# Kernel optimization log

Hardware: AMD Instinct MI355X
Metric: run time of the kernel (lower is better)

## Reference

```python
import math
import jax, jax.numpy as jnp
import numpy as np

B, N, T, C, H = 16, 307, 24, 128, 8
D = C // H
FACTOR = 5
S = min(FACTOR * int(np.ceil(np.log(T))), T)   # sample_k (U_part) = 20
U = S                                          # n_top u = 20


def _pos_emb(t_len, c):
    pos = jnp.arange(t_len, dtype=jnp.float32)[:, None]
    div = jnp.exp(jnp.arange(0, c, 2, dtype=jnp.float32) * (-math.log(10000.0) / c))
    pe = jnp.zeros((t_len, c), dtype=jnp.float32)
    pe = pe.at[:, 0::2].set(jnp.sin(pos * div))
    pe = pe.at[:, 1::2].set(jnp.cos(pos * div))
    return pe  # [T, C]


def _layernorm(x, g, b, eps=1e-5):
    m = x.mean(-1, keepdims=True)
    v = ((x - m) ** 2).mean(-1, keepdims=True)
    return (x - m) / jnp.sqrt(v + eps) * g + b


def _forward(query, time_encoder, index_sample,
             emb_minute, emb_hour, emb_weekday, emb_month, emb_year,
             Wq, Wk, Wv, Wo, bo, ff_w1, ff_b1, ff_w2, ff_b2,
             ln1_g, ln1_b, ln2_g, ln2_b):
    # DataEmbedding: x + positional + temporal (dropout = identity in eval)
    pe = _pos_emb(T, C)                                   # [T, C]
    te = (emb_minute[time_encoder[..., 0]] + emb_hour[time_encoder[..., 1]]
          + emb_weekday[time_encoder[..., 2]] + emb_month[time_encoder[..., 3]]
          + emb_year[time_encoder[..., 4]])               # [B, T, C]
    x = query + pe[None, None, :, :] + te[:, None, :, :]  # [B, N, T, C]

    # QKV projections -> [B, H, N, T, D]
    def proj(inp, W):
        return (inp @ W).reshape(B, N, T, H, D).transpose(0, 3, 1, 2, 4)
    Q, K, V = proj(x, Wq), proj(x, Wk), proj(x, Wv)

    # ProbSparse: sample S keys per query position
    K_samp = K[:, :, :, index_sample, :]                  # [B, H, N, T, S, D]
    QK_samp = jnp.einsum('bhntd,bhntsd->bhnts', Q, K_samp)
    M = QK_samp.max(-1) - QK_samp.sum(-1) / S             # [B, H, N, T]
    _, M_top = jax.lax.top_k(M, U)                        # [B, H, N, U]

    Q_red = jnp.take_along_axis(Q, M_top[..., None], axis=3)  # [B, H, N, U, D]
    scores = jnp.einsum('bhnud,bhntd->bhnut', Q_red, K) * (1.0 / math.sqrt(D))
    attn = jax.nn.softmax(scores, axis=-1)
    upd = jnp.einsum('bhnut,bhntd->bhnud', attn, V)       # [B, H, N, U, D]

    # initial context = mean over T, then scatter-update top-u query rows
    ctx = jnp.broadcast_to(V.mean(axis=3, keepdims=True), V.shape)
    ctx = ctx.at[jnp.arange(B)[:, None, None, None],
                 jnp.arange(H)[None, :, None, None],
                 jnp.arange(N)[None, None, :, None],
                 M_top].set(upd)

    ctx = ctx.transpose(0, 2, 3, 1, 4).reshape(B, N, T, C)
    att_out = ctx @ Wo + bo

    x1 = _layernorm(att_out + x, ln1_g, ln1_b)
    ff = jax.nn.relu(x1 @ ff_w1 + ff_b1) @ ff_w2 + ff_b2
    out = _layernorm(ff + x1, ln2_g, ln2_b)
    return out


def setup_inputs() -> dict:
    key = jax.random.key(0)
    ks = jax.random.split(key, 32)
    def nrm(i, shape, s=0.02):
        return jax.random.normal(ks[i], shape, dtype=jnp.float32) * s
    inp = {
        'value': jax.random.normal(ks[0], (B, N, T, C), dtype=jnp.float32),
        'key_in': jax.random.normal(ks[1], (B, N, T, C), dtype=jnp.float32),
        'query': jax.random.normal(ks[2], (B, N, T, C), dtype=jnp.float32),
        't': 1,
        'time_encoder': jax.random.randint(ks[3], (B, T, 5), 0, 10),
        'index_sample': jax.random.randint(ks[4], (T, S), 0, T),
        'emb_minute': nrm(5, (70, C), 1.0), 'emb_hour': nrm(6, (30, C), 1.0),
        'emb_weekday': nrm(7, (10, C), 1.0), 'emb_month': nrm(8, (40, C), 1.0),
        'emb_year': nrm(9, (400, C), 1.0),
        'Wq': nrm(10, (C, C)), 'Wk': nrm(11, (C, C)), 'Wv': nrm(12, (C, C)),
        'Wo': nrm(13, (C, C)), 'bo': jnp.zeros((C,), jnp.float32),
        'ff_w1': nrm(14, (C, 4 * C)), 'ff_b1': jnp.zeros((4 * C,), jnp.float32),
        'ff_w2': nrm(15, (4 * C, C)), 'ff_b2': jnp.zeros((C,), jnp.float32),
        'ln1_g': jnp.ones((C,), jnp.float32), 'ln1_b': jnp.zeros((C,), jnp.float32),
        'ln2_g': jnp.ones((C,), jnp.float32), 'ln2_b': jnp.zeros((C,), jnp.float32),
    }
    return inp


def reference(value, key_in, query, t, time_encoder, index_sample,
              emb_minute, emb_hour, emb_weekday, emb_month, emb_year,
              Wq, Wk, Wv, Wo, bo, ff_w1, ff_b1, ff_w2, ff_b2,
              ln1_g, ln1_b, ln2_g, ln2_b):
    # value, key_in, t are accepted but unused, matching the torch module
    return _forward(query, time_encoder, index_sample,
                    emb_minute, emb_hour, emb_weekday, emb_month, emb_year,
                    Wq, Wk, Wv, Wo, bo, ff_w1, ff_b1, ff_w2, ff_b2,
                    ln1_g, ln1_b, ln2_g, ln2_b)
```

## Files before the change

### kernel.cpp

```cpp
#include <hip/hip_runtime.h>
#include <hip/hip_bf16.h>
#include <cmath>

namespace {
constexpr int B_ = 16, N_ = 307, T_ = 24, C_ = 128, H_ = 8, D_ = 16, S_ = 20, U_ = 20;
constexpr int NROW = B_ * N_ * T_;
constexpr int NX = NROW * C_;
constexpr int TEPE_N = B_ * T_ * C_;
constexpr int FF = 4 * C_;
constexpr int BM = 32;
constexpr int NBLK_MM = NROW / BM;
constexpr int BMT = 64;
constexpr int NBLK_T = NROW / BMT;
constexpr int NUNIT = B_ * H_ * N_;
}

typedef __attribute__((ext_vector_type(8))) short short8;
typedef __attribute__((ext_vector_type(4))) short short4_;
typedef __attribute__((ext_vector_type(4))) float f32x4;

__device__ inline short f2bf(float v) {
    union { float f; unsigned u; } a; a.f = v;
    unsigned r = a.u + 0x7fff + ((a.u >> 16) & 1);
    return (short)(r >> 16);
}
__device__ inline float bf2f(short s) {
    return __bfloat162float(*(const __hip_bfloat16*)&s);
}

__global__ void k_tepe(const int* __restrict__ te,
                       const float* __restrict__ e_min, const float* __restrict__ e_hr,
                       const float* __restrict__ e_wd, const float* __restrict__ e_mo,
                       const float* __restrict__ e_yr, float* __restrict__ tepe,
                       const int* __restrict__ idxs, unsigned char* __restrict__ cntg) {
    int i = blockIdx.x * blockDim.x + threadIdx.x;
    if (i < TEPE_N) {
        int c = i & (C_ - 1);
        int bt = i >> 7;
        int t = bt % T_;
        const int* enc = te + bt * 5;
        float v = e_min[enc[0] * C_ + c] + e_hr[enc[1] * C_ + c] + e_wd[enc[2] * C_ + c]
                + e_mo[enc[3] * C_ + c] + e_yr[enc[4] * C_ + c];
        float ang = (float)t * expf(-(float)(c & ~1) * (9.210340371976184f / 128.0f));
        v += (c & 1) ? cosf(ang) : sinf(ang);
        tepe[i] = v;
    }
    if (blockIdx.x == 0) {
        __shared__ int scnt[T_ * 32];
        for (int j = threadIdx.x; j < T_ * 32; j += 256) scnt[j] = 0;
        __syncthreads();
        for (int j = threadIdx.x; j < T_ * S_; j += 256) {
            int t = j / S_;
            atomicAdd(&scnt[t * 32 + idxs[j]], 1);
        }
        __syncthreads();
        for (int j = threadIdx.x; j < 192; j += 256) {
            unsigned v = (unsigned)scnt[4 * j] | ((unsigned)scnt[4 * j + 1] << 8)
                       | ((unsigned)scnt[4 * j + 2] << 16) | ((unsigned)scnt[4 * j + 3] << 24);
            ((unsigned*)cntg)[j] = v;
        }
    }
}

__global__ void k_wcvt_qkv(const float* __restrict__ Wq, const float* __restrict__ Wk,
                           const float* __restrict__ Wv, short* __restrict__ wqkvf) {
    int i = blockIdx.x * 256 + threadIdx.x;
    int tile = i >> 9, l = (i >> 3) & 63, e = i & 7;
    int c_tile = tile >> 2, ks = tile & 3;
    int c_all = c_tile * 16 + (l & 15);
    int k = ks * 32 + (l >> 4) * 8 + e;
    int m = c_all >> 7, c = c_all & (C_ - 1);
    const float* W = (m == 0) ? Wq : (m == 1) ? Wk : Wv;
    wqkvf[i] = f2bf(W[k * C_ + c]);
}

__global__ void k_wcvt2(const float* __restrict__ w1, const float* __restrict__ w2,
                        const float* __restrict__ Wo,
                        short* __restrict__ w1f, short* __restrict__ w2f,
                        short* __restrict__ wof) {
    int i = blockIdx.x * 256 + threadIdx.x;
    if (i < C_ * FF) {
        int tile = i >> 9, l = (i >> 3) & 63, e = i & 7;
        int jtile = tile >> 2, ks = tile & 3;
        int j = jtile * 16 + (l & 15);
        int k = ks * 32 + (l >> 4) * 8 + e;
        w1f[i] = f2bf(w1[k * FF + j]);
    } else if (i < 2 * C_ * FF) {
        int i2 = i - C_ * FF;
        int tile = i2 >> 9, l = (i2 >> 3) & 63, e = i2 & 7;
        int c_tile = tile >> 4, ks = tile & 15;
        int c = c_tile * 16 + (l & 15);
        int j = ks * 32 + (l >> 4) * 8 + e;
        w2f[i2] = f2bf(w2[j * C_ + c]);
    } else {
        int i3 = i - 2 * C_ * FF;
        int tile = i3 >> 9, l = (i3 >> 3) & 63, e = i3 & 7;
        int c_tile = tile >> 2, ks = tile & 3;
        int c = c_tile * 16 + (l & 15);
        int k = ks * 32 + (l >> 4) * 8 + e;
        wof[i3] = f2bf(Wo[k * C_ + c]);
    }
}

__global__ __launch_bounds__(256) void k_qkv_mfma(
    const float* __restrict__ query, const float* __restrict__ tepe,
    const short* __restrict__ wqkvf,
    short* __restrict__ Q, short* __restrict__ K, short* __restrict__ V) {
    __shared__ __align__(16) short xs[BM * C_];
    int tid = threadIdx.x;
    int r0 = blockIdx.x * BM;
    {
        int row = tid >> 3;
        int cb = (tid & 7) * 16;
        int gr = r0 + row;
        int t = gr % T_;
        int b = gr / (N_ * T_);
        const float* qsrc = query + (size_t)gr * C_ + cb;
        const float* tsrc = tepe + (size_t)(b * T_ + t) * C_ + cb;
        int swz0 = (row & 7) << 3;
#pragma unroll
        for (int i = 0; i < 4; i++) {
            float4 q4 = *(const float4*)(qsrc + 4 * i);
            float4 t4 = *(const float4*)(tsrc + 4 * i);
            short4_ sv;
            sv.x = f2bf(q4.x + t4.x); sv.y = f2bf(q4.y + t4.y);
            sv.z = f2bf(q4.z + t4.z); sv.w = f2bf(q4.w + t4.w);
            *(short4_*)&xs[(row * C_ + cb + 4 * i) ^ swz0] = sv;
        }
    }
    __syncthreads();
    int w = tid >> 6, l = tid & 63;
    int lr = l & 15, lk = l >> 4;
    int swz = (lr & 7) << 3;
    short8 bx[2][4];
#pragma unroll
    for (int rt = 0; rt < 2; rt++)
#pragma unroll
        for (int ks = 0; ks < 4; ks++)
            bx[rt][ks] = *(const short8*)&xs[((rt * 16 + lr) * C_ + ks * 32 + lk * 8) ^ swz];
    size_t base[2];
#pragma unroll
    for (int rt = 0; rt < 2; rt++) {
        int gr = r0 + rt * 16 + lr;
        int t = gr % T_;
        int n = (gr / T_) % N_;
        int b = gr / (N_ * T_);
        base[rt] = ((size_t)b * H_ * N_ + n) * (T_ * D_) + t * D_;
    }
#pragma unroll
    for (int jt = 0; jt < 6; jt++) {
        int ctile = w * 6 + jt;
        const short* ap = wqkvf + (size_t)ctile * 2048 + l * 8;
        short8 acur[4];
#pragma unroll
        for (int ks = 0; ks < 4; ks++) acur[ks] = *(const short8*)(ap + ks * 512);
        f32x4 acc[2] = {{0.f, 0.f, 0.f, 0.f}, {0.f, 0.f, 0.f, 0.f}};
#pragma unroll
        for (int ks = 0; ks < 4; ks++) {
#pragma unroll
            for (int rt = 0; rt < 2; rt++)
                acc[rt] = __builtin_amdgcn_mfma_f32_16x16x32_bf16(acur[ks], bx[rt][ks], acc[rt], 0, 0, 0);
        }
        int c0 = ctile * 16 + lk * 4;
        int m = c0 >> 7;
        int c = c0 & (C_ - 1);
        int h = c >> 4, d = c & 15;
        short* dst = (m == 0) ? Q : (m == 1) ? K : V;
#pragma unroll
        for (int rt = 0; rt < 2; rt++) {
            short4_ sv;
            sv.x = f2bf(acc[rt][0]); sv.y = f2bf(acc[rt][1]);
            sv.z = f2bf(acc[rt][2]); sv.w = f2bf(acc[rt][3]);
            *(short4_*)&dst[base[rt] + (size_t)h * (N_ * T_ * D_) + d] = sv;
        }
    }
}

__global__ __launch_bounds__(256) void k_attn(
    const short* __restrict__ Q, const short* __restrict__ K, const short* __restrict__ V,
    const unsigned char* __restrict__ cntg, short* __restrict__ ctx) {
    __shared__ __align__(16) short Qbf[4][32 * 24], Kbf[4][32 * 24];
    __shared__ __align__(16) short Vt[4][16 * 40];
    __shared__ __align__(16) short Pbf[4][32 * 40];
    __shared__ unsigned char cntS[T_ * 32];
    __shared__ float Mv[4][T_];
    __shared__ int keepS[4][T_];
    __shared__ float meanVs[4][D_];
    int tid = threadIdx.x;
    int wid = tid >> 6, l = tid & 63;
    int e = blockIdx.x * 4 + wid;
    const short* qb = Q + (size_t)e * (T_ * D_);
    const short* kb = K + (size_t)e * (T_ * D_);
    const short* vb = V + (size_t)e * (T_ * D_);
    if (l < 48) {
        int t = l >> 1, hf = l & 1;
        *(short8*)&Qbf[wid][t * 24 + hf * 8] = *(const short8*)(qb + t * 16 + hf * 8);
        *(short8*)&Kbf[wid][t * 24 + hf * 8] = *(const short8*)(kb + t * 16 + hf * 8);
    }
    for (int i = l; i < 96; i += 64) {
        int t = i >> 2, c4 = i & 3;
        short4_ v = *(const short4_*)(vb + t * 16 + c4 * 4);
        Vt[wid][(c4 * 4 + 0) * 40 + t] = v.x;
        Vt[wid][(c4 * 4 + 1) * 40 + t] = v.y;
        Vt[wid][(c4 * 4 + 2) * 40 + t] = v.z;
        Vt[wid][(c4 * 4 + 3) * 40 + t] = v.w;
    }
    for (int i = l; i < 128; i += 64) {
        int d = i >> 3, c = 24 + (i & 7);
        Vt[wid][d * 40 + c] = 0;
    }
    if (tid < 192) ((int*)cntS)[tid] = ((const int*)cntg)[tid];
    __syncthreads();
    if (l >= 48) {
        int d = l - 48;
        float s = 0.f;
        for (int t = 0; t < T_; t++) s += bf2f(Vt[wid][d * 40 + t]);
        meanVs[wid][d] = s * (1.0f / T_);
    }
    int lr = l & 15, lk = l >> 4;
    short8 zz = {};
    short8 kf0 = zz, kf1 = zz, qf0 = zz, qf1 = zz;
    if (lk < 2) {
        kf0 = *(const short8*)&Kbf[wid][lr * 24 + lk * 8];
        kf1 = *(const short8*)&Kbf[wid][(16 + lr) * 24 + lk * 8];
        qf0 = *(const short8*)&Qbf[wid][lr * 24 + lk * 8];
        qf1 = *(const short8*)&Qbf[wid][(16 + lr) * 24 + lk * 8];
    }
    f32x4 zf = {0.f, 0.f, 0.f, 0.f};
    f32x4 s00 = __builtin_amdgcn_mfma_f32_16x16x32_bf16(kf0, qf0, zf, 0, 0, 0);
    f32x4 s01 = __builtin_amdgcn_mfma_f32_16x16x32_bf16(kf1, qf0, zf, 0, 0, 0);
    f32x4 s10 = __builtin_amdgcn_mfma_f32_16x16x32_bf16(kf0, qf1, zf, 0, 0, 0);
    f32x4 s11 = __builtin_amdgcn_mfma_f32_16x16x32_bf16(kf1, qf1, zf, 0, 0, 0);
#pragma unroll
    for (int rt = 0; rt < 2; rt++) {
        int t = rt * 16 + lr;
        int tt = (t < T_) ? t : 0;
        f32x4 c0 = rt ? s10 : s00;
        f32x4 c1 = rt ? s11 : s01;
        float mx = -1e30f, sm = 0.f;
#pragma unroll
        for (int i = 0; i < 4; i++) {
            int cA = cntS[tt * 32 + lk * 4 + i];
            if (cA) { mx = fmaxf(mx, c0[i]); sm += (float)cA * c0[i]; }
        }
        if (lk < 2) {
#pragma unroll
            for (int i = 0; i < 4; i++) {
                int cB = cntS[tt * 32 + 16 + lk * 4 + i];
                if (cB) { mx = fmaxf(mx, c1[i]); sm += (float)cB * c1[i]; }
            }
        }
        mx = fmaxf(mx, __shfl_xor(mx, 16));
        mx = fmaxf(mx, __shfl_xor(mx, 32));
        sm += __shfl_xor(sm, 16);
        sm += __shfl_xor(sm, 32);
        if (lk == 0 && t < T_) Mv[wid][t] = mx - sm * (1.0f / S_);
    }
    __syncthreads();
    if (l < T_) {
        float mt = Mv[wid][l];
        int cnt2 = 0;
        for (int t2 = 0; t2 < T_; t2++) {
            float m2 = Mv[wid][t2];
            cnt2 += (m2 > mt) || (m2 == mt && t2 < l);
        }
        keepS[wid][l] = (cnt2 < U_) ? 1 : 0;
    }
#pragma unroll
    for (int rt = 0; rt < 2; rt++) {
        f32x4 c0 = rt ? s10 : s00;
        f32x4 c1 = rt ? s11 : s01;
        float lm = fmaxf(fmaxf(c0[0], c0[1]), fmaxf(c0[2], c0[3]));
        if (lk < 2) lm = fmaxf(lm, fmaxf(fmaxf(c1[0], c1[1]), fmaxf(c1[2], c1[3])));
        lm = fmaxf(lm, __shfl_xor(lm, 16));
        lm = fmaxf(lm, __shfl_xor(lm, 32));
        float e0[4], e1[4];
        float ls = 0.f;
#pragma unroll
        for (int i = 0; i < 4; i++) { e0[i] = __expf(0.25f * (c0[i] - lm)); ls += e0[i]; }
#pragma unroll
        for (int i = 0; i < 4; i++) { e1[i] = (lk < 2) ? __expf(0.25f * (c1[i] - lm)) : 0.f; ls += e1[i]; }
        ls += __shfl_xor(ls, 16);
        ls += __shfl_xor(ls, 32);
        float inv = 1.0f / ls;
        short4_ w0, w1;
        w0.x = f2bf(e0[0] * inv); w0.y = f2bf(e0[1] * inv);
        w0.z = f2bf(e0[2] * inv); w0.w = f2bf(e0[3] * inv);
        w1.x = f2bf(e1[0] * inv); w1.y = f2bf(e1[1] * inv);
        w1.z = f2bf(e1[2] * inv); w1.w = f2bf(e1[3] * inv);
        int trow = rt * 16 + lr;
        *(short4_*)&Pbf[wid][trow * 40 + lk * 4] = w0;
        *(short4_*)&Pbf[wid][trow * 40 + 16 + lk * 4] = w1;
    }
    __syncthreads();
    short8 vf = *(const short8*)&Vt[wid][lr * 40 + lk * 8];
    short8 pf0 = *(const short8*)&Pbf[wid][lr * 40 + lk * 8];
    short8 pf1 = *(const short8*)&Pbf[wid][(16 + lr) * 40 + lk * 8];
    f32x4 u0 = __builtin_amdgcn_mfma_f32_16x16x32_bf16(vf, pf0, zf, 0, 0, 0);
    f32x4 u1 = __builtin_amdgcn_mfma_f32_16x16x32_bf16(vf, pf1, zf, 0, 0, 0);
    int b = e / (H_ * N_);
    int h = (e / N_) % H_;
    int n = e % N_;
    float4 mv4 = *(const float4*)&meanVs[wid][lk * 4];
#pragma unroll
    for (int rt = 0; rt < 2; rt++) {
        int t = rt * 16 + lr;
        if (t < T_) {
            f32x4 u = rt ? u1 : u0;
            float4 o;
            if (keepS[wid][t]) { o.x = u[0]; o.y = u[1]; o.z = u[2]; o.w = u[3]; }
            else o = mv4;
            short4_ sv;
            sv.x = f2bf(o.x); sv.y = f2bf(o.y); sv.z = f2bf(o.z); sv.w = f2bf(o.w);
            *(short4_*)&ctx[((size_t)(b * N_ + n) * T_ + t) * C_ + h * D_ + lk * 4] = sv;
        }
    }
}

__global__ __launch_bounds__(512, 4) void k_tail(
    const short* __restrict__ ctx, const short* __restrict__ wof, const float* __restrict__ bo,
    const float* __restrict__ query, const float* __restrict__ tepe,
    const float* __restrict__ g1, const float* __restrict__ b1,
    const short* __restrict__ w1f, const float* __restrict__ b1f,
    const short* __restrict__ w2f, const float* __restrict__ b2f,
    const float* __restrict__ g2, const float* __restrict__ b2ln,
    float* __restrict__ out) {
    __shared__ __align__(16) char smem[81920];
    short* cbf = (short*)smem;
    float (*xf)[132] = (float(*)[132])(smem + 16384);
    short* x1bf = (short*)(smem + 65536);
    short* hbf = (short*)smem;
    float (*yf)[132] = (float(*)[132])smem;
    int tid = threadIdx.x;
    int r0 = blockIdx.x * BMT;
    {
        int row = tid >> 3;
        int cb = (tid & 7) * 16;
        int gr = r0 + row;
        int t = gr % T_;
        int b = gr / (N_ * T_);
        const short* csrc = ctx + (size_t)gr * C_ + cb;
        const float* qsrc = query + (size_t)gr * C_ + cb;
        const float* tsrc = tepe + (size_t)(b * T_ + t) * C_ + cb;
        int swz0 = (row & 7) << 3;
        *(short8*)&cbf[(row * C_ + cb) ^ swz0] = *(const short8*)csrc;
        *(short8*)&cbf[(row * C_ + cb + 8) ^ swz0] = *(const short8*)(csrc + 8);
#pragma unroll
        for (int i = 0; i < 4; i++) {
            float4 q4 = *(const float4*)(qsrc + 4 * i);
            float4 t4 = *(const float4*)(tsrc + 4 * i);
            float4 xr;
            xr.x = q4.x + t4.x; xr.y = q4.y + t4.y;
            xr.z = q4.z + t4.z; xr.w = q4.w + t4.w;
            *(float4*)&xf[row][cb + 4 * i] = xr;
        }
    }
    __syncthreads();
    int w = tid >> 6, l = tid & 63;
    int lr = l & 15, lk = l >> 4;
    int swz = (lr & 7) << 3;
    {
        const short* ap = wof + (size_t)w * 2048 + l * 8;
        f32x4 acc[4] = {{0.f, 0.f, 0.f, 0.f}, {0.f, 0.f, 0.f, 0.f},
                        {0.f, 0.f, 0.f, 0.f}, {0.f, 0.f, 0.f, 0.f}};
#pragma unroll
        for (int ks = 0; ks < 4; ks++) {
            short8 aw = *(const short8*)(ap + ks * 512);
#pragma unroll
            for (int rt = 0; rt < 4; rt++) {
                short8 bc = *(const short8*)&cbf[((rt * 16 + lr) * C_ + ks * 32 + lk * 8) ^ swz];
                acc[rt] = __builtin_amdgcn_mfma_f32_16x16x32_bf16(aw, bc, acc[rt], 0, 0, 0);
            }
        }
        int cc = w * 16 + lk * 4;
        float4 bias = *(const float4*)(bo + cc);
#pragma unroll
        for (int rt = 0; rt < 4; rt++) {
            int rr = rt * 16 + lr;
            float4 res = *(const float4*)&xf[rr][cc];
            float4 o;
            o.x = acc[rt][0] + bias.x + res.x;
            o.y = acc[rt][1] + bias.y + res.y;
            o.z = acc[rt][2] + bias.z + res.z;
            o.w = acc[rt][3] + bias.w + res.w;
            *(float4*)&xf[rr][cc] = o;
        }
    }
    __syncthreads();
    {
        int r = tid >> 3;
        int q = tid & 7;
        int cb = q * 16;
        float vals[16];
        float s = 0.f;
#pragma unroll
        for (int i = 0; i < 16; i++) { vals[i] = xf[r][cb + i]; s += vals[i]; }
        s += __shfl_xor(s, 1, 8);
        s += __shfl_xor(s, 2, 8);
        s += __shfl_xor(s, 4, 8);
        float mean = s * (1.f / C_);
        float vv = 0.f;
#pragma unroll
        for (int i = 0; i < 16; i++) { float d = vals[i] - mean; vv += d * d; }
        vv += __shfl_xor(vv, 1, 8);
        vv += __shfl_xor(vv, 2, 8);
        vv += __shfl_xor(vv, 4, 8);
        float rstd = rsqrtf(vv * (1.f / C_) + 1e-5f);
        short8 o0, o1;
#pragma unroll
        for (int i = 0; i < 8; i++) {
            o0[i] = f2bf((vals[i] - mean) * rstd * g1[cb + i] + b1[cb + i]);
            o1[i] = f2bf((vals[8 + i] - mean) * rstd * g1[cb + 8 + i] + b1[cb + 8 + i]);
        }
        int swz0 = (r & 7) << 3;
        *(short8*)&x1bf[(r * C_ + cb) ^ swz0] = o0;
        *(short8*)&x1bf[(r * C_ + cb + 8) ^ swz0] = o1;
    }
    __syncthreads();
    {
        short8 bx[4][4];
#pragma unroll
        for (int rt = 0; rt < 4; rt++)
#pragma unroll
            for (int ks = 0; ks < 4; ks++)
                bx[rt][ks] = *(const short8*)&x1bf[((rt * 16 + lr) * C_ + ks * 32 + lk * 8) ^ swz];
#pragma unroll
        for (int jt = 0; jt < 4; jt++) {
            int jtile = w * 4 + jt;
            const short* ap = w1f + (size_t)jtile * 2048 + l * 8;
            short8 acur[4];
#pragma unroll
            for (int ks = 0; ks < 4; ks++) acur[ks] = *(const short8*)(ap + ks * 512);
            f32x4 acc[4] = {{0.f, 0.f, 0.f, 0.f}, {0.f, 0.f, 0.f, 0.f},
                            {0.f, 0.f, 0.f, 0.f}, {0.f, 0.f, 0.f, 0.f}};
#pragma unroll
            for (int ks = 0; ks < 4; ks++) {
#pragma unroll
                for (int rt = 0; rt < 4; rt++)
                    acc[rt] = __builtin_amdgcn_mfma_f32_16x16x32_bf16(acur[ks], bx[rt][ks], acc[rt], 0, 0, 0);
            }
            int j0 = jtile * 16 + lk * 4;
            float4 bias = *(const float4*)(b1f + j0);
#pragma unroll
            for (int rt = 0; rt < 4; rt++) {
                int rr = rt * 16 + lr;
                short4_ hv;
                hv.x = f2bf(fmaxf(acc[rt][0] + bias.x, 0.f));
                hv.y = f2bf(fmaxf(acc[rt][1] + bias.y, 0.f));
                hv.z = f2bf(fmaxf(acc[rt][2] + bias.z, 0.f));
                hv.w = f2bf(fmaxf(acc[rt][3] + bias.w, 0.f));
                *(short4_*)&hbf[(rr * FF + j0) ^ swz] = hv;
            }
        }
    }
    __syncthreads();
    f32x4 acc2[4] = {{0.f, 0.f, 0.f, 0.f}, {0.f, 0.f, 0.f, 0.f},
                     {0.f, 0.f, 0.f, 0.f}, {0.f, 0.f, 0.f, 0.f}};
#pragma unroll 4
    for (int ks = 0; ks < 16; ks++) {
        short8 aw = *(const short8*)(w2f + ((size_t)(w * 16 + ks)) * 512 + l * 8);
#pragma unroll
        for (int rt = 0; rt < 4; rt++) {
            short8 hx = *(const short8*)&hbf[((rt * 16 + lr) * FF + ks * 32 + lk * 8) ^ swz];
            acc2[rt] = __builtin_amdgcn_mfma_f32_16x16x32_bf16(aw, hx, acc2[rt], 0, 0, 0);
        }
    }
    int cc = w * 16 + lk * 4;
    float4 bias2 = *(const float4*)(b2f + cc);
    float4 res[4];
#pragma unroll
    for (int rt = 0; rt < 4; rt++) {
        short4_ rb = *(const short4_*)&x1bf[((rt * 16 + lr) * C_ + cc) ^ swz];
        res[rt].x = bf2f(rb.x); res[rt].y = bf2f(rb.y);
        res[rt].z = bf2f(rb.z); res[rt].w = bf2f(rb.w);
    }
    __syncthreads();
#pragma unroll
    for (int rt = 0; rt < 4; rt++) {
        float4 o;
        o.x = acc2[rt][0] + bias2.x + res[rt].x;
        o.y = acc2[rt][1] + bias2.y + res[rt].y;
        o.z = acc2[rt][2] + bias2.z + res[rt].z;
        o.w = acc2[rt][3] + bias2.w + res[rt].w;
        *(float4*)&yf[rt * 16 + lr][cc] = o;
    }
    __syncthreads();
    {
        int r = tid >> 3;
        int q = tid & 7;
        int cb = q * 16;
        float vals[16];
        float s = 0.f;
#pragma unroll
        for (int i = 0; i < 16; i++) { vals[i] = yf[r][cb + i]; s += vals[i]; }
        s += __shfl_xor(s, 1, 8);
        s += __shfl_xor(s, 2, 8);
        s += __shfl_xor(s, 4, 8);
        float mean = s * (1.f / C_);
        float vv = 0.f;
#pragma unroll
        for (int i = 0; i < 16; i++) { float d = vals[i] - mean; vv += d * d; }
        vv += __shfl_xor(vv, 1, 8);
        vv += __shfl_xor(vv, 2, 8);
        vv += __shfl_xor(vv, 4, 8);
        float rstd = rsqrtf(vv * (1.f / C_) + 1e-5f);
        float* op = out + (size_t)(r0 + r) * C_ + cb;
#pragma unroll
        for (int i4 = 0; i4 < 4; i4++) {
            float4 gv = *(const float4*)(g2 + cb + 4 * i4);
            float4 bv = *(const float4*)(b2ln + cb + 4 * i4);
            float4 ov;
            ov.x = (vals[4 * i4 + 0] - mean) * rstd * gv.x + bv.x;
            ov.y = (vals[4 * i4 + 1] - mean) * rstd * gv.y + bv.y;
            ov.z = (vals[4 * i4 + 2] - mean) * rstd * gv.z + bv.z;
            ov.w = (vals[4 * i4 + 3] - mean) * rstd * gv.w + bv.w;
            *(float4*)(op + 4 * i4) = ov;
        }
    }
}

extern "C" void kernel_launch(void* const* d_in, const int* in_sizes, int n_in,
                              void* d_out, int out_size, void* d_ws, size_t ws_size,
                              hipStream_t stream) {
    const float* query = (const float*)d_in[2];
    const int* time_enc = (const int*)d_in[4];
    const int* index_sample = (const int*)d_in[5];
    const float* e_min = (const float*)d_in[6];
    const float* e_hr  = (const float*)d_in[7];
    const float* e_wd  = (const float*)d_in[8];
    const float* e_mo  = (const float*)d_in[9];
    const float* e_yr  = (const float*)d_in[10];
    const float* Wq = (const float*)d_in[11];
    const float* Wk = (const float*)d_in[12];
    const float* Wv = (const float*)d_in[13];
    const float* Wo = (const float*)d_in[14];
    const float* bo = (const float*)d_in[15];
    const float* ffw1 = (const float*)d_in[16];
    const float* ffb1 = (const float*)d_in[17];
    const float* ffw2 = (const float*)d_in[18];
    const float* ffb2 = (const float*)d_in[19];
    const float* ln1g = (const float*)d_in[20];
    const float* ln1b = (const float*)d_in[21];
    const float* ln2g = (const float*)d_in[22];
    const float* ln2b = (const float*)d_in[23];

    float* ws = (float*)d_ws;
    float* tepe = ws;
    float* region1 = ws + TEPE_N;
    float* region2 = region1 + NX;
    float* region3 = region2 + NX;
    float* region4 = region3 + NX;

    short* Qb = (short*)region1;
    short* Kb = (short*)region2;
    short* Vb = (short*)region3;
    short* ctxb = (short*)region4;
    short* wqkvf = (short*)region4 + NX;
    unsigned char* cntg = (unsigned char*)((short*)region4 + NX + 49152);
    short* w1f = (short*)region2;
    short* w2f = w1f + C_ * FF;
    short* wof = w2f + C_ * FF;

    k_tepe<<<dim3(TEPE_N / 256), dim3(256), 0, stream>>>(
        time_enc, e_min, e_hr, e_wd, e_mo, e_yr, tepe, index_sample, cntg);
    k_wcvt_qkv<<<dim3(384 * C_ / 256), dim3(256), 0, stream>>>(Wq, Wk, Wv, wqkvf);
    k_qkv_mfma<<<dim3(NBLK_MM), dim3(256), 0, stream>>>(
        query, tepe, wqkvf, Qb, Kb, Vb);
    k_attn<<<dim3(NUNIT / 4), dim3(256), 0, stream>>>(
        Qb, Kb, Vb, cntg, ctxb);
    k_wcvt2<<<dim3((2 * C_ * FF + C_ * C_) / 256), dim3(256), 0, stream>>>(
        ffw1, ffw2, Wo, w1f, w2f, wof);
    k_tail<<<dim3(NBLK_T), dim3(512), 0, stream>>>(
        ctxb, wof, bo, query, tepe, ln1g, ln1b,
        w1f, ffb1, w2f, ffb2, ln2g, ln2b, (float*)d_out);
}
```

Measured before the change: 170.6 us.

## Split FFN hidden dimension into two halves to shrink LDS and raise occupancy

```diff
diff --git a/kernel.cpp b/kernel.cpp
--- a/kernel.cpp
+++ b/kernel.cpp
@@ -317,7 +317,7 @@
     }
 }
 
-__global__ __launch_bounds__(512, 4) void k_tail(
+__global__ __launch_bounds__(512, 6) void k_tail(
     const short* __restrict__ ctx, const short* __restrict__ wof, const float* __restrict__ bo,
     const float* __restrict__ query, const float* __restrict__ tepe,
     const float* __restrict__ g1, const float* __restrict__ b1,
@@ -325,12 +325,12 @@
     const short* __restrict__ w2f, const float* __restrict__ b2f,
     const float* __restrict__ g2, const float* __restrict__ b2ln,
     float* __restrict__ out) {
-    __shared__ __align__(16) char smem[81920];
-    short* cbf = (short*)smem;
-    float (*xf)[132] = (float(*)[132])(smem + 16384);
-    short* x1bf = (short*)(smem + 65536);
+    __shared__ __align__(16) char smem[51200];
+    float (*xf)[136] = (float(*)[136])smem;
     short* hbf = (short*)smem;
-    float (*yf)[132] = (float(*)[132])smem;
+    float (*yf)[136] = (float(*)[136])smem;
+    short* cbf = (short*)(smem + 34816);
+    short* x1bf = (short*)(smem + 34816);
     int tid = threadIdx.x;
     int r0 = blockIdx.x * BMT;
     {
@@ -417,72 +417,72 @@
         *(short8*)&x1bf[(r * C_ + cb + 8) ^ swz0] = o1;
     }
     __syncthreads();
-    {
-        short8 bx[4][4];
-#pragma unroll
-        for (int rt = 0; rt < 4; rt++)
-#pragma unroll
-            for (int ks = 0; ks < 4; ks++)
-                bx[rt][ks] = *(const short8*)&x1bf[((rt * 16 + lr) * C_ + ks * 32 + lk * 8) ^ swz];
-#pragma unroll
-        for (int jt = 0; jt < 4; jt++) {
-            int jtile = w * 4 + jt;
-            const short* ap = w1f + (size_t)jtile * 2048 + l * 8;
-            short8 acur[4];
-#pragma unroll
-            for (int ks = 0; ks < 4; ks++) acur[ks] = *(const short8*)(ap + ks * 512);
-            f32x4 acc[4] = {{0.f, 0.f, 0.f, 0.f}, {0.f, 0.f, 0.f, 0.f},
-                            {0.f, 0.f, 0.f, 0.f}, {0.f, 0.f, 0.f, 0.f}};
-#pragma unroll
-            for (int ks = 0; ks < 4; ks++) {
-#pragma unroll
-                for (int rt = 0; rt < 4; rt++)
-                    acc[rt] = __builtin_amdgcn_mfma_f32_16x16x32_bf16(acur[ks], bx[rt][ks], acc[rt], 0, 0, 0);
-            }
-            int j0 = jtile * 16 + lk * 4;
-            float4 bias = *(const float4*)(b1f + j0);
-#pragma unroll
-            for (int rt = 0; rt < 4; rt++) {
-                int rr = rt * 16 + lr;
-                short4_ hv;
-                hv.x = f2bf(fmaxf(acc[rt][0] + bias.x, 0.f));
-                hv.y = f2bf(fmaxf(acc[rt][1] + bias.y, 0.f));
-                hv.z = f2bf(fmaxf(acc[rt][2] + bias.z, 0.f));
-                hv.w = f2bf(fmaxf(acc[rt][3] + bias.w, 0.f));
-                *(short4_*)&hbf[(rr * FF + j0) ^ swz] = hv;
-            }
-        }
-    }
-    __syncthreads();
     f32x4 acc2[4] = {{0.f, 0.f, 0.f, 0.f}, {0.f, 0.f, 0.f, 0.f},
                      {0.f, 0.f, 0.f, 0.f}, {0.f, 0.f, 0.f, 0.f}};
-#pragma unroll 4
-    for (int ks = 0; ks < 16; ks++) {
-        short8 aw = *(const short8*)(w2f + ((size_t)(w * 16 + ks)) * 512 + l * 8);
+    for (int p = 0; p < 2; p++) {
+        {
+            short8 bx[4][4];
+#pragma unroll
+            for (int rt = 0; rt < 4; rt++)
+#pragma unroll
+                for (int ks = 0; ks < 4; ks++)
+                    bx[rt][ks] = *(const short8*)&x1bf[((rt * 16 + lr) * C_ + ks * 32 + lk * 8) ^ swz];
+#pragma unroll
+            for (int jt = 0; jt < 2; jt++) {
+                int jtile = p * 16 + w * 2 + jt;
+                const short* ap = w1f + (size_t)jtile * 2048 + l * 8;
+                short8 acur[4];
+#pragma unroll
+                for (int ks = 0; ks < 4; ks++) acur[ks] = *(const short8*)(ap + ks * 512);
+                f32x4 acc[4] = {{0.f, 0.f, 0.f, 0.f}, {0.f, 0.f, 0.f, 0.f},
+                                {0.f, 0.f, 0.f, 0.f}, {0.f, 0.f, 0.f, 0.f}};
+#pragma unroll
+                for (int ks = 0; ks < 4; ks++) {
+#pragma unroll
+                    for (int rt = 0; rt < 4; rt++)
+                        acc[rt] = __builtin_amdgcn_mfma_f32_16x16x32_bf16(acur[ks], bx[rt][ks], acc[rt], 0, 0, 0);
+                }
+                int j0g = jtile * 16 + lk * 4;
+                int j0l = (w * 2 + jt) * 16 + lk * 4;
+                float4 bias = *(const float4*)(b1f + j0g);
+#pragma unroll
+                for (int rt = 0; rt < 4; rt++) {
+                    int rr = rt * 16 + lr;
+                    short4_ hv;
+                    hv.x = f2bf(fmaxf(acc[rt][0] + bias.x, 0.f));
+                    hv.y = f2bf(fmaxf(acc[rt][1] + bias.y, 0.f));
+                    hv.z = f2bf(fmaxf(acc[rt][2] + bias.z, 0.f));
+                    hv.w = f2bf(fmaxf(acc[rt][3] + bias.w, 0.f));
+                    *(short4_*)&hbf[(rr * 256 + j0l) ^ swz] = hv;
+                }
+            }
+        }
+        __syncthreads();
+#pragma unroll 2
+        for (int ks = 0; ks < 8; ks++) {
+            short8 aw = *(const short8*)(w2f + ((size_t)(w * 16 + p * 8 + ks)) * 512 + l * 8);
+#pragma unroll
+            for (int rt = 0; rt < 4; rt++) {
+                short8 hx = *(const short8*)&hbf[((rt * 16 + lr) * 256 + ks * 32 + lk * 8) ^ swz];
+                acc2[rt] = __builtin_amdgcn_mfma_f32_16x16x32_bf16(aw, hx, acc2[rt], 0, 0, 0);
+            }
+        }
+        __syncthreads();
+    }
+    {
+        int cc = w * 16 + lk * 4;
+        float4 bias2 = *(const float4*)(b2f + cc);
 #pragma unroll
         for (int rt = 0; rt < 4; rt++) {
-            short8 hx = *(const short8*)&hbf[((rt * 16 + lr) * FF + ks * 32 + lk * 8) ^ swz];
-            acc2[rt] = __builtin_amdgcn_mfma_f32_16x16x32_bf16(aw, hx, acc2[rt], 0, 0, 0);
-        }
-    }
-    int cc = w * 16 + lk * 4;
-    float4 bias2 = *(const float4*)(b2f + cc);
-    float4 res[4];
-#pragma unroll
-    for (int rt = 0; rt < 4; rt++) {
-        short4_ rb = *(const short4_*)&x1bf[((rt * 16 + lr) * C_ + cc) ^ swz];
-        res[rt].x = bf2f(rb.x); res[rt].y = bf2f(rb.y);
-        res[rt].z = bf2f(rb.z); res[rt].w = bf2f(rb.w);
-    }
-    __syncthreads();
-#pragma unroll
-    for (int rt = 0; rt < 4; rt++) {
-        float4 o;
-        o.x = acc2[rt][0] + bias2.x + res[rt].x;
-        o.y = acc2[rt][1] + bias2.y + res[rt].y;
-        o.z = acc2[rt][2] + bias2.z + res[rt].z;
-        o.w = acc2[rt][3] + bias2.w + res[rt].w;
-        *(float4*)&yf[rt * 16 + lr][cc] = o;
+            int rr = rt * 16 + lr;
+            short4_ rb = *(const short4_*)&x1bf[(rr * C_ + cc) ^ swz];
+            float4 o;
+            o.x = acc2[rt][0] + bias2.x + bf2f(rb.x);
+            o.y = acc2[rt][1] + bias2.y + bf2f(rb.y);
+            o.z = acc2[rt][2] + bias2.z + bf2f(rb.z);
+            o.w = acc2[rt][3] + bias2.w + bf2f(rb.w);
+            *(float4*)&yf[rr][cc] = o;
+        }
     }
     __syncthreads();
     {
```

Result: slower. 229.2 us (+34.4%).

## Restructure tail kernel to 4 waves with register-resident Wo+LN1 and prefetched weights

Applied to the files above, without the earlier changes.

```diff
diff --git a/kernel.cpp b/kernel.cpp
--- a/kernel.cpp
+++ b/kernel.cpp
@@ -317,7 +317,7 @@
     }
 }
 
-__global__ __launch_bounds__(512, 4) void k_tail(
+__global__ __launch_bounds__(256, 4) void k_tail(
     const short* __restrict__ ctx, const short* __restrict__ wof, const float* __restrict__ bo,
     const float* __restrict__ query, const float* __restrict__ tepe,
     const float* __restrict__ g1, const float* __restrict__ b1,
@@ -326,96 +326,81 @@
     const float* __restrict__ g2, const float* __restrict__ b2ln,
     float* __restrict__ out) {
     __shared__ __align__(16) char smem[81920];
-    short* cbf = (short*)smem;
-    float (*xf)[132] = (float(*)[132])(smem + 16384);
-    short* x1bf = (short*)(smem + 65536);
     short* hbf = (short*)smem;
     float (*yf)[132] = (float(*)[132])smem;
+    short* x1bf = (short*)(smem + 65536);
     int tid = threadIdx.x;
     int r0 = blockIdx.x * BMT;
-    {
-        int row = tid >> 3;
-        int cb = (tid & 7) * 16;
-        int gr = r0 + row;
-        int t = gr % T_;
-        int b = gr / (N_ * T_);
-        const short* csrc = ctx + (size_t)gr * C_ + cb;
-        const float* qsrc = query + (size_t)gr * C_ + cb;
-        const float* tsrc = tepe + (size_t)(b * T_ + t) * C_ + cb;
-        int swz0 = (row & 7) << 3;
-        *(short8*)&cbf[(row * C_ + cb) ^ swz0] = *(const short8*)csrc;
-        *(short8*)&cbf[(row * C_ + cb + 8) ^ swz0] = *(const short8*)(csrc + 8);
-#pragma unroll
-        for (int i = 0; i < 4; i++) {
-            float4 q4 = *(const float4*)(qsrc + 4 * i);
-            float4 t4 = *(const float4*)(tsrc + 4 * i);
-            float4 xr;
-            xr.x = q4.x + t4.x; xr.y = q4.y + t4.y;
-            xr.z = q4.z + t4.z; xr.w = q4.w + t4.w;
-            *(float4*)&xf[row][cb + 4 * i] = xr;
-        }
-    }
-    __syncthreads();
     int w = tid >> 6, l = tid & 63;
     int lr = l & 15, lk = l >> 4;
     int swz = (lr & 7) << 3;
+    int myloc = w * 16 + lr;
+    int gr = r0 + myloc;
+    int t = gr % T_;
+    int b = gr / (N_ * T_);
+    const short* csrc = ctx + (size_t)gr * C_;
+    short8 bc[4];
+#pragma unroll
+    for (int ks = 0; ks < 4; ks++)
+        bc[ks] = *(const short8*)(csrc + ks * 32 + lk * 8);
+    const float* qsrc = query + (size_t)gr * C_;
+    const float* tsrc = tepe + (size_t)(b * T_ + t) * C_;
+    float4 xres[8];
+#pragma unroll
+    for (int ct = 0; ct < 8; ct++) {
+        float4 q4 = *(const float4*)(qsrc + ct * 16 + lk * 4);
+        float4 t4 = *(const float4*)(tsrc + ct * 16 + lk * 4);
+        xres[ct].x = q4.x + t4.x; xres[ct].y = q4.y + t4.y;
+        xres[ct].z = q4.z + t4.z; xres[ct].w = q4.w + t4.w;
+    }
+#pragma unroll
+    for (int ct = 0; ct < 8; ct++) {
+        f32x4 acc = {0.f, 0.f, 0.f, 0.f};
+#pragma unroll
+        for (int ks = 0; ks < 4; ks++) {
+            short8 aw = *(const short8*)(wof + (size_t)(ct * 4 + ks) * 512 + l * 8);
+            acc = __builtin_amdgcn_mfma_f32_16x16x32_bf16(aw, bc[ks], acc, 0, 0, 0);
+        }
+        float4 bo4 = *(const float4*)(bo + ct * 16 + lk * 4);
+        xres[ct].x += acc[0] + bo4.x;
+        xres[ct].y += acc[1] + bo4.y;
+        xres[ct].z += acc[2] + bo4.z;
+        xres[ct].w += acc[3] + bo4.w;
+    }
     {
-        const short* ap = wof + (size_t)w * 2048 + l * 8;
-        f32x4 acc[4] = {{0.f, 0.f, 0.f, 0.f}, {0.f, 0.f, 0.f, 0.f},
-                        {0.f, 0.f, 0.f, 0.f}, {0.f, 0.f, 0.f, 0.f}};
-#pragma unroll
-        for (int ks = 0; ks < 4; ks++) {
-            short8 aw = *(const short8*)(ap + ks * 512);
-#pragma unroll
-            for (int rt = 0; rt < 4; rt++) {
-                short8 bc = *(const short8*)&cbf[((rt * 16 + lr) * C_ + ks * 32 + lk * 8) ^ swz];
-                acc[rt] = __builtin_amdgcn_mfma_f32_16x16x32_bf16(aw, bc, acc[rt], 0, 0, 0);
-            }
-        }
-        int cc = w * 16 + lk * 4;
-        float4 bias = *(const float4*)(bo + cc);
-#pragma unroll
-        for (int rt = 0; rt < 4; rt++) {
-            int rr = rt * 16 + lr;
-            float4 res = *(const float4*)&xf[rr][cc];
-            float4 o;
-            o.x = acc[rt][0] + bias.x + res.x;
-            o.y = acc[rt][1] + bias.y + res.y;
-            o.z = acc[rt][2] + bias.z + res.z;
-            o.w = acc[rt][3] + bias.w + res.w;
-            *(float4*)&xf[rr][cc] = o;
-        }
-    }
-    __syncthreads();
-    {
-        int r = tid >> 3;
-        int q = tid & 7;
-        int cb = q * 16;
-        float vals[16];
         float s = 0.f;
 #pragma unroll
-        for (int i = 0; i < 16; i++) { vals[i] = xf[r][cb + i]; s += vals[i]; }
-        s += __shfl_xor(s, 1, 8);
-        s += __shfl_xor(s, 2, 8);
-        s += __shfl_xor(s, 4, 8);
+        for (int ct = 0; ct < 8; ct++)
+            s += xres[ct].x + xres[ct].y + xres[ct].z + xres[ct].w;
+        s += __shfl_xor(s, 16);
+        s += __shfl_xor(s, 32);
         float mean = s * (1.f / C_);
         float vv = 0.f;
 #pragma unroll
-        for (int i = 0; i < 16; i++) { float d = vals[i] - mean; vv += d * d; }
-        vv += __shfl_xor(vv, 1, 8);
-        vv += __shfl_xor(vv, 2, 8);
-        vv += __shfl_xor(vv, 4, 8);
+        for (int ct = 0; ct < 8; ct++) {
+            float dx = xres[ct].x - mean, dy = xres[ct].y - mean;
+            float dz = xres[ct].z - mean, dw = xres[ct].w - mean;
+            vv += dx * dx + dy * dy + dz * dz + dw * dw;
+        }
+        vv += __shfl_xor(vv, 16);
+        vv += __shfl_xor(vv, 32);
         float rstd = rsqrtf(vv * (1.f / C_) + 1e-5f);
-        short8 o0, o1;
-#pragma unroll
-        for (int i = 0; i < 8; i++) {
-            o0[i] = f2bf((vals[i] - mean) * rstd * g1[cb + i] + b1[cb + i]);
-            o1[i] = f2bf((vals[8 + i] - mean) * rstd * g1[cb + 8 + i] + b1[cb + 8 + i]);
-        }
-        int swz0 = (r & 7) << 3;
-        *(short8*)&x1bf[(r * C_ + cb) ^ swz0] = o0;
-        *(short8*)&x1bf[(r * C_ + cb + 8) ^ swz0] = o1;
-    }
+#pragma unroll
+        for (int ct = 0; ct < 8; ct++) {
+            float4 gv = *(const float4*)(g1 + ct * 16 + lk * 4);
+            float4 bv = *(const float4*)(b1 + ct * 16 + lk * 4);
+            short4_ xv;
+            xv.x = f2bf((xres[ct].x - mean) * rstd * gv.x + bv.x);
+            xv.y = f2bf((xres[ct].y - mean) * rstd * gv.y + bv.y);
+            xv.z = f2bf((xres[ct].z - mean) * rstd * gv.z + bv.z);
+            xv.w = f2bf((xres[ct].w - mean) * rstd * gv.w + bv.w);
+            *(short4_*)&x1bf[(myloc * C_ + ct * 16 + lk * 4) ^ swz] = xv;
+        }
+    }
+    const short* w1base = w1f + (size_t)(w * 8) * 2048 + l * 8;
+    short8 acur[4];
+#pragma unroll
+    for (int ks = 0; ks < 4; ks++) acur[ks] = *(const short8*)(w1base + ks * 512);
     __syncthreads();
     {
         short8 bx[4][4];
@@ -425,68 +410,97 @@
             for (int ks = 0; ks < 4; ks++)
                 bx[rt][ks] = *(const short8*)&x1bf[((rt * 16 + lr) * C_ + ks * 32 + lk * 8) ^ swz];
 #pragma unroll
-        for (int jt = 0; jt < 4; jt++) {
-            int jtile = w * 4 + jt;
-            const short* ap = w1f + (size_t)jtile * 2048 + l * 8;
-            short8 acur[4];
-#pragma unroll
-            for (int ks = 0; ks < 4; ks++) acur[ks] = *(const short8*)(ap + ks * 512);
-            f32x4 acc[4] = {{0.f, 0.f, 0.f, 0.f}, {0.f, 0.f, 0.f, 0.f},
-                            {0.f, 0.f, 0.f, 0.f}, {0.f, 0.f, 0.f, 0.f}};
+        for (int jt = 0; jt < 8; jt++) {
+            short8 anxt[4];
+            if (jt < 7) {
+#pragma unroll
+                for (int ks = 0; ks < 4; ks++)
+                    anxt[ks] = *(const short8*)(w1base + (size_t)(jt + 1) * 2048 + ks * 512);
+            }
+            f32x4 a1[4] = {{0.f, 0.f, 0.f, 0.f}, {0.f, 0.f, 0.f, 0.f},
+                           {0.f, 0.f, 0.f, 0.f}, {0.f, 0.f, 0.f, 0.f}};
 #pragma unroll
             for (int ks = 0; ks < 4; ks++) {
 #pragma unroll
                 for (int rt = 0; rt < 4; rt++)
-                    acc[rt] = __builtin_amdgcn_mfma_f32_16x16x32_bf16(acur[ks], bx[rt][ks], acc[rt], 0, 0, 0);
+                    a1[rt] = __builtin_amdgcn_mfma_f32_16x16x32_bf16(acur[ks], bx[rt][ks], a1[rt], 0, 0, 0);
             }
-            int j0 = jtile * 16 + lk * 4;
-            float4 bias = *(const float4*)(b1f + j0);
+            int j0 = (w * 8 + jt) * 16 + lk * 4;
+            float4 b1v = *(const float4*)(b1f + j0);
 #pragma unroll
             for (int rt = 0; rt < 4; rt++) {
                 int rr = rt * 16 + lr;
                 short4_ hv;
-                hv.x = f2bf(fmaxf(acc[rt][0] + bias.x, 0.f));
-                hv.y = f2bf(fmaxf(acc[rt][1] + bias.y, 0.f));
-                hv.z = f2bf(fmaxf(acc[rt][2] + bias.z, 0.f));
-                hv.w = f2bf(fmaxf(acc[rt][3] + bias.w, 0.f));
+                hv.x = f2bf(fmaxf(a1[rt][0] + b1v.x, 0.f));
+                hv.y = f2bf(fmaxf(a1[rt][1] + b1v.y, 0.f));
+                hv.z = f2bf(fmaxf(a1[rt][2] + b1v.z, 0.f));
+                hv.w = f2bf(fmaxf(a1[rt][3] + b1v.w, 0.f));
                 *(short4_*)&hbf[(rr * FF + j0) ^ swz] = hv;
             }
-        }
-    }
-    __syncthreads();
-    f32x4 acc2[4] = {{0.f, 0.f, 0.f, 0.f}, {0.f, 0.f, 0.f, 0.f},
-                     {0.f, 0.f, 0.f, 0.f}, {0.f, 0.f, 0.f, 0.f}};
+#pragma unroll
+            for (int ks = 0; ks < 4; ks++) acur[ks] = anxt[ks];
+        }
+    }
+    short8 aA[2];
+#pragma unroll
+    for (int ct = 0; ct < 2; ct++)
+        aA[ct] = *(const short8*)(w2f + (size_t)((w * 2 + ct) * 16) * 512 + l * 8);
+    __syncthreads();
+    f32x4 acc2[2][4] = {{{0.f, 0.f, 0.f, 0.f}, {0.f, 0.f, 0.f, 0.f},
+                         {0.f, 0.f, 0.f, 0.f}, {0.f, 0.f, 0.f, 0.f}},
+                        {{0.f, 0.f, 0.f, 0.f}, {0.f, 0.f, 0.f, 0.f},
+                         {0.f, 0.f, 0.f, 0.f}, {0.f, 0.f, 0.f, 0.f}}};
 #pragma unroll 4
     for (int ks = 0; ks < 16; ks++) {
-        short8 aw = *(const short8*)(w2f + ((size_t)(w * 16 + ks)) * 512 + l * 8);
+        short8 aB[2];
+        if (ks < 15) {
+#pragma unroll
+            for (int ct = 0; ct < 2; ct++)
+                aB[ct] = *(const short8*)(w2f + (size_t)((w * 2 + ct) * 16 + ks + 1) * 512 + l * 8);
+        }
+        short8 hx[4];
+#pragma unroll
+        for (int rt = 0; rt < 4; rt++)
+            hx[rt] = *(const short8*)&hbf[((rt * 16 + lr) * FF + ks * 32 + lk * 8) ^ swz];
+#pragma unroll
+        for (int ct = 0; ct < 2; ct++)
+#pragma unroll
+            for (int rt = 0; rt < 4; rt++)
+                acc2[ct][rt] = __builtin_amdgcn_mfma_f32_16x16x32_bf16(aA[ct], hx[rt], acc2[ct][rt], 0, 0, 0);
+#pragma unroll
+        for (int ct = 0; ct < 2; ct++) aA[ct] = aB[ct];
+    }
+    float4 res[2][4], b2v[2];
+#pragma unroll
+    for (int ct = 0; ct < 2; ct++) {
+        int cc = (w * 2 + ct) * 16 + lk * 4;
+        b2v[ct] = *(const float4*)(b2f + cc);
 #pragma unroll
         for (int rt = 0; rt < 4; rt++) {
-            short8 hx = *(const short8*)&hbf[((rt * 16 + lr) * FF + ks * 32 + lk * 8) ^ swz];
-            acc2[rt] = __builtin_amdgcn_mfma_f32_16x16x32_bf16(aw, hx, acc2[rt], 0, 0, 0);
-        }
-    }
-    int cc = w * 16 + lk * 4;
-    float4 bias2 = *(const float4*)(b2f + cc);
-    float4 res[4];
-#pragma unroll
-    for (int rt = 0; rt < 4; rt++) {
-        short4_ rb = *(const short4_*)&x1bf[((rt * 16 + lr) * C_ + cc) ^ swz];
-        res[rt].x = bf2f(rb.x); res[rt].y = bf2f(rb.y);
-        res[rt].z = bf2f(rb.z); res[rt].w = bf2f(rb.w);
-    }
-    __syncthreads();
-#pragma unroll
-    for (int rt = 0; rt < 4; rt++) {
-        float4 o;
-        o.x = acc2[rt][0] + bias2.x + res[rt].x;
-        o.y = acc2[rt][1] + bias2.y + res[rt].y;
-        o.z = acc2[rt][2] + bias2.z + res[rt].z;
-        o.w = acc2[rt][3] + bias2.w + res[rt].w;
-        *(float4*)&yf[rt * 16 + lr][cc] = o;
-    }
-    __syncthreads();
-    {
-        int r = tid >> 3;
+            short4_ rb = *(const short4_*)&x1bf[((rt * 16 + lr) * C_ + cc) ^ swz];
+            res[ct][rt].x = bf2f(rb.x); res[ct][rt].y = bf2f(rb.y);
+            res[ct][rt].z = bf2f(rb.z); res[ct][rt].w = bf2f(rb.w);
+        }
+    }
+    __syncthreads();
+#pragma unroll
+    for (int ct = 0; ct < 2; ct++) {
+        int cc = (w * 2 + ct) * 16 + lk * 4;
+#pragma unroll
+        for (int rt = 0; rt < 4; rt++) {
+            int rr = rt * 16 + lr;
+            float4 o;
+            o.x = acc2[ct][rt][0] + b2v[ct].x + res[ct][rt].x;
+            o.y = acc2[ct][rt][1] + b2v[ct].y + res[ct][rt].y;
+            o.z = acc2[ct][rt][2] + b2v[ct].z + res[ct][rt].z;
+            o.w = acc2[ct][rt][3] + b2v[ct].w + res[ct][rt].w;
+            *(float4*)&yf[rr][cc] = o;
+        }
+    }
+    __syncthreads();
+#pragma unroll
+    for (int half = 0; half < 2; half++) {
+        int r = (tid >> 3) + half * 32;
         int q = tid & 7;
         int cb = q * 16;
         float vals[16];
@@ -570,7 +584,7 @@
         Qb, Kb, Vb, cntg, ctxb);
     k_wcvt2<<<dim3((2 * C_ * FF + C_ * C_) / 256), dim3(256), 0, stream>>>(
         ffw1, ffw2, Wo, w1f, w2f, wof);
-    k_tail<<<dim3(NBLK_T), dim3(512), 0, stream>>>(
+    k_tail<<<dim3(NBLK_T), dim3(256), 0, stream>>>(
         ctxb, wof, bo, query, tepe, ln1g, ln1b,
         w1f, ffb1, w2f, ffb2, ln2g, ln2b, (float*)d_out);
 }
```

New measurement: 174.0 us. +2.0%, slower.
